# Performance work log

Measured on AMD Instinct MI355X. Metric: run time of the kernel, lower is better.

Reference implementation:

```python
import jax, jax.numpy as jnp
import numpy as np

CUTOFF_UPPER = 4.5
EYE3 = jnp.eye(3, dtype=jnp.float32)


def tensor_norm(t):
    return (t ** 2).sum((-2, -1))


def decompose_tensor(X):
    # X: [N, C, 3, 3]
    tr_mean = jnp.trace(X, axis1=-2, axis2=-1) / 3.0
    I = tr_mean[..., None, None] * EYE3
    Xt = jnp.swapaxes(X, -2, -1)
    A = 0.5 * (X - Xt)
    S = 0.5 * (X + Xt) - I
    return I, A, S


def chan_linear(T, W, b):
    # torch: Linear applied over the channel axis after permute(0,2,3,1)
    # T: [N, C, 3, 3], W: [C, C], b: [C]
    return jnp.einsum('nkij,ck->ncij', T, W) + b[None, :, None, None]


def setup_inputs() -> dict:
    key = jax.random.key(0)
    ks = jax.random.split(key, 16)
    Np1, H, R, E = 20001, 128, 64, 200000
    X = jax.random.normal(ks[0], (Np1, H, 3, 3), dtype=jnp.float32)
    edge_index = jax.random.randint(ks[1], (2, E), 0, Np1)
    edge_weight = jax.random.uniform(ks[2], (E,), dtype=jnp.float32) * CUTOFF_UPPER
    edge_attr = jax.random.normal(ks[3], (E, R), dtype=jnp.float32)
    s = lambda fin: 1.0 / np.sqrt(fin)
    W1 = jax.random.uniform(ks[4], (3, H, H), minval=-s(H), maxval=s(H), dtype=jnp.float32)
    b1 = jax.random.uniform(ks[5], (3, H), minval=-s(H), maxval=s(H), dtype=jnp.float32)
    W2a = jax.random.uniform(ks[6], (H, R), minval=-s(R), maxval=s(R), dtype=jnp.float32)
    b2a = jax.random.uniform(ks[7], (H,), minval=-s(R), maxval=s(R), dtype=jnp.float32)
    W2b = jax.random.uniform(ks[8], (2 * H, H), minval=-s(H), maxval=s(H), dtype=jnp.float32)
    b2b = jax.random.uniform(ks[9], (2 * H,), minval=-s(H), maxval=s(H), dtype=jnp.float32)
    W2c = jax.random.uniform(ks[10], (3 * H, 2 * H), minval=-s(2 * H), maxval=s(2 * H), dtype=jnp.float32)
    b2c = jax.random.uniform(ks[11], (3 * H,), minval=-s(2 * H), maxval=s(2 * H), dtype=jnp.float32)
    W3 = jax.random.uniform(ks[12], (3, H, H), minval=-s(H), maxval=s(H), dtype=jnp.float32)
    b3 = jax.random.uniform(ks[13], (3, H), minval=-s(H), maxval=s(H), dtype=jnp.float32)
    return dict(X=X, edge_index=edge_index, edge_weight=edge_weight, edge_attr=edge_attr,
                W1=W1, b1=b1, W2a=W2a, b2a=b2a, W2b=W2b, b2b=b2b, W2c=W2c, b2c=b2c, W3=W3, b3=b3)


def reference(X, edge_index, edge_weight, edge_attr, W1, b1, W2a, b2a, W2b, b2b, W2c, b2c, W3, b3):
    Np1, H = X.shape[0], X.shape[1]
    act = jax.nn.silu
    X = X / (tensor_norm(X) + 1.0)[..., None, None]
    I, A, S = decompose_tensor(X)
    I = chan_linear(I, W1[0], b1[0])
    A = chan_linear(A, W1[1], b1[1])
    S = chan_linear(S, W1[2], b1[2])
    Y = I + A + S
    h = act(edge_attr @ W2a.T + b2a)
    h = act(h @ W2b.T + b2b)
    h = act(h @ W2c.T + b2c)  # [E, 3H]
    C = 0.5 * (jnp.cos(edge_weight * (jnp.pi / CUTOFF_UPPER)) + 1.0)
    C = C * (edge_weight < CUTOFF_UPPER).astype(C.dtype)
    ea = (h * C[:, None]).reshape(h.shape[0], H, 3)
    dst, src = edge_index[0], edge_index[1]

    def mp(factor, T):
        msg = factor[:, :, None, None] * T[src]  # [E, H, 3, 3]
        return jax.ops.segment_sum(msg, dst, num_segments=Np1)

    msg = mp(ea[..., 0], I) + mp(ea[..., 1], A) + mp(ea[..., 2], S)
    new_features = jnp.matmul(msg, Y) + jnp.matmul(Y, msg)  # O(3) branch
    I, A, S = decompose_tensor(new_features)
    norm = (tensor_norm(I + A + S) + 1.0)[..., None, None]
    I, A, S = I / norm, A / norm, S / norm
    I = chan_linear(I, W3[0], b3[0])
    A = chan_linear(A, W3[1], b3[1])
    S = chan_linear(S, W3[2], b3[2])
    dX = I + A + S
    return X + dX + jnp.matmul(dX, dX)
```

## Files before the change

kernel.cpp:

```cpp
#include <hip/hip_runtime.h>
#include <math.h>
#include <stdint.h>

typedef unsigned short u16;
typedef __attribute__((ext_vector_type(8))) short short8;
typedef __attribute__((ext_vector_type(4))) float floatx4;

__device__ __forceinline__ float b2f(u16 u){
  union{unsigned int i; float f;} v; v.i = ((unsigned int)u)<<16; return v.f;
}
__device__ __forceinline__ u16 f2b(float f){
  union{unsigned int i; float f;} v; v.f = f;
  unsigned int r = (v.i + 0x7FFFu + ((v.i>>16)&1u))>>16;
  return (u16)r;
}
__device__ __forceinline__ float ldx(const void* p, size_t i, int isb){
  return isb ? b2f(((const u16*)p)[i]) : ((const float*)p)[i];
}
__device__ __forceinline__ void gll16(const u16* g, u16* l){
  __builtin_amdgcn_global_load_lds(
      (const __attribute__((address_space(1))) unsigned int*)(g),
      (__attribute__((address_space(3))) unsigned int*)(l), 16, 0, 0);
}

__global__ void k_sniff(const void* __restrict__ X, int* __restrict__ flag)
{
  __shared__ int cnt;
  if (threadIdx.x==0) cnt = 0;
  __syncthreads();
  int c = 0;
  for (int t = threadIdx.x; t < 512; t += 256){
    unsigned int u = ((const u16*)X)[2*t];
    int e = (u >> 7) & 0xFF;
    if (e >= 110 && e <= 139) c++;
  }
  atomicAdd(&cnt, c);
  __syncthreads();
  if (threadIdx.x==0) *flag = (cnt > 300) ? 1 : 0;
}

__global__ __launch_bounds__(256) void k_zero(float* __restrict__ p, int n)
{
  int i = blockIdx.x*256 + threadIdx.x;
  if (i < n) p[i] = 0.f;
}
__global__ __launch_bounds__(256) void k_zero_int(int* __restrict__ p, int n)
{
  int i = blockIdx.x*256 + threadIdx.x;
  if (i < n) p[i] = 0;
}

__global__ __launch_bounds__(256) void k_hist(
    const int* __restrict__ ei, int* __restrict__ counts, int E)
{
  int e = blockIdx.x*256 + threadIdx.x;
  if (e < E) atomicAdd(&counts[ei[e]], 1);
}
__global__ __launch_bounds__(256) void k_scan(
    const int* __restrict__ counts, int* __restrict__ rowptr,
    int* __restrict__ fill, int N)
{
  __shared__ int sm[256];
  int tid = threadIdx.x;
  int per = (N + 255) >> 8;
  int lo = tid*per; if (lo > N) lo = N;
  int hi = lo + per; if (hi > N) hi = N;
  int s = 0;
  for (int i = lo; i < hi; i++) s += counts[i];
  sm[tid] = s;
  __syncthreads();
  for (int off=1; off<256; off<<=1){
    int t = (tid >= off) ? sm[tid-off] : 0;
    __syncthreads();
    sm[tid] += t;
    __syncthreads();
  }
  int run = sm[tid] - s;
  for (int i = lo; i < hi; i++){
    int v = counts[i];
    rowptr[i] = run; fill[i] = run;
    run += v;
  }
  if (tid == 0) rowptr[N] = sm[255];
}
__global__ __launch_bounds__(256) void k_scatter(
    const int* __restrict__ ei, int* __restrict__ fill,
    int* __restrict__ eorder, int E)
{
  int e = blockIdx.x*256 + threadIdx.x;
  if (e >= E) return;
  int d = ei[e];
  int pos = atomicAdd(&fill[d], 1);
  eorder[pos] = e;
}

__global__ __launch_bounds__(256) void k_cvt_weights(
    const void* __restrict__ W1, const void* __restrict__ W3,
    const void* __restrict__ W2a, const void* __restrict__ W2b,
    const void* __restrict__ W2c, u16* __restrict__ out,
    const int* __restrict__ dflag)
{
  int isb = *dflag;
  int i = blockIdx.x*256 + threadIdx.x;
  if (i >= 237568) return;
  float v;
  if (i < 49152)        v = ldx(W1, i, isb);
  else if (i < 98304)   v = ldx(W3, i-49152, isb);
  else if (i < 106496)  v = ldx(W2a, i-98304, isb);
  else if (i < 139264)  v = ldx(W2b, i-106496, isb);
  else {
    int j = i - 139264;
    int r = j >> 8, c = j & 255;
    v = ldx(W2c, (size_t)((r & 127)*3 + (r >> 7))*256 + c, isb);
  }
  out[i] = f2b(v);
}
__global__ __launch_bounds__(256) void k_cvt_biases(
    const void* __restrict__ b2a, const void* __restrict__ b2b,
    const void* __restrict__ b2c, float* __restrict__ out,
    const int* __restrict__ dflag)
{
  int isb = *dflag;
  int i = blockIdx.x*256 + threadIdx.x;
  if (i < 128) out[i] = ldx(b2a, i, isb);
  else if (i < 384) out[i] = ldx(b2b, i-128, isb);
  else if (i < 768){ int c = i-384; out[i] = ldx(b2c, (c&127)*3 + (c>>7), isb); }
}
__global__ __launch_bounds__(256) void k_perm_eatt(
    const void* __restrict__ eatt, const int* __restrict__ eorder,
    u16* __restrict__ dst, int E, const int* __restrict__ dflag)
{
  int isb = *dflag;
  int row = blockIdx.x*4 + (threadIdx.x >> 6);
  int c = threadIdx.x & 63;
  if (row >= E) return;
  int e = eorder[row];
  dst[(size_t)row*64 + c] = f2b(ldx(eatt, (size_t)e*64 + c, isb));
}

__global__ __launch_bounds__(256) void k_decompose(
    const void* __restrict__ X, u16* __restrict__ Di, u16* __restrict__ Da,
    u16* __restrict__ Ds, int NH, const int* __restrict__ dflag)
{
  int tid = blockIdx.x*256 + threadIdx.x;
  if (tid >= NH) return;
  int isb = *dflag;
  int n = tid >> 7, k = tid & 127;
  float x[9]; float nrm = 0.f;
#pragma unroll
  for (int i=0;i<9;i++){ x[i]=ldx(X,(size_t)tid*9+i,isb); nrm += x[i]*x[i]; }
  float inv = 1.0f/(nrm+1.0f);
#pragma unroll
  for (int i=0;i<9;i++) x[i]*=inv;
  float i0 = (x[0]+x[4]+x[8])*(1.0f/3.0f);
  Di[tid] = f2b(i0);
  size_t ab = ((size_t)n*3)*128 + k;
  Da[ab      ] = f2b(0.5f*(x[1]-x[3]));
  Da[ab + 128] = f2b(0.5f*(x[2]-x[6]));
  Da[ab + 256] = f2b(0.5f*(x[5]-x[7]));
  size_t sb = ((size_t)n*6)*128 + k;
  Ds[sb      ] = f2b(x[0]-i0);
  Ds[sb + 128] = f2b(0.5f*(x[1]+x[3]));
  Ds[sb + 256] = f2b(0.5f*(x[2]+x[6]));
  Ds[sb + 384] = f2b(x[4]-i0);
  Ds[sb + 512] = f2b(0.5f*(x[5]+x[7]));
  Ds[sb + 640] = f2b(x[8]-i0);
}

__global__ __launch_bounds__(256) void k_mfma_gemm(
    const u16* __restrict__ A, const u16* __restrict__ B,
    const float* __restrict__ bias, const float* __restrict__ rowscale,
    u16* __restrict__ C, int M, int Ncol, int K, int flags)
{
  __shared__ u16 As[4096];
  __shared__ u16 Bs[4096];
  const int tid = threadIdx.x;
  const int lane = tid & 63, l15 = lane & 15, q = lane >> 4;
  const int wid = tid >> 6, wm = wid & 1, wn = wid >> 1;
  const int n0 = blockIdx.x * 128, m0 = blockIdx.y * 128;

  const int srow = wid*32 + (lane >> 2);
  const int qsrc = (lane & 3) ^ ((lane >> 3) & 3);
  int ar0 = m0 + srow;      if (ar0 >= M) ar0 = M-1;
  int ar1 = m0 + srow + 16; if (ar1 >= M) ar1 = M-1;
  const u16* aSrc0 = A + (size_t)ar0*K + qsrc*8;
  const u16* aSrc1 = A + (size_t)ar1*K + qsrc*8;
  const u16* bSrc0 = B + (size_t)(n0 + srow)*K + qsrc*8;
  const u16* bSrc1 = B + (size_t)(n0 + srow + 16)*K + qsrc*8;
  u16* aDst0 = &As[wid*1024];  u16* aDst1 = &As[wid*1024 + 512];
  u16* bDst0 = &Bs[wid*1024];  u16* bDst1 = &Bs[wid*1024 + 512];

  floatx4 acc[4][4];
#pragma unroll
  for (int i=0;i<4;i++)
#pragma unroll
    for (int j=0;j<4;j++) acc[i][j] = (floatx4)0.f;

  const int qsw  = ((q ^ ((l15 >> 1) & 3)) << 3);
  const int aBase = (wm*64 + l15)*32 + qsw;
  const int bBase = (wn*64 + l15)*32 + qsw;

  for (int k0 = 0; k0 < K; k0 += 32){
    gll16(aSrc0 + k0, aDst0);
    gll16(aSrc1 + k0, aDst1);
    gll16(bSrc0 + k0, bDst0);
    gll16(bSrc1 + k0, bDst1);
    __syncthreads();
    short8 av[4], bv[4];
#pragma unroll
    for (int mt=0; mt<4; mt++)
      av[mt] = *reinterpret_cast<const short8*>(&As[aBase + mt*512]);
#pragma unroll
    for (int nt=0; nt<4; nt++)
      bv[nt] = *reinterpret_cast<const short8*>(&Bs[bBase + nt*512]);
#pragma unroll
    for (int mt=0; mt<4; mt++)
#pragma unroll
      for (int nt=0; nt<4; nt++)
        acc[mt][nt] = __builtin_amdgcn_mfma_f32_16x16x32_bf16(av[mt], bv[nt], acc[mt][nt], 0, 0, 0);
    __syncthreads();
  }

  float biasv[4];
#pragma unroll
  for (int nt=0; nt<4; nt++)
    biasv[nt] = bias ? bias[n0 + wn*64 + nt*16 + l15] : 0.f;
#pragma unroll
  for (int mt=0; mt<4; mt++){
#pragma unroll
    for (int reg=0; reg<4; reg++){
      int row = m0 + wm*64 + mt*16 + q*4 + reg;
      if (row >= M) continue;
      float rs = (flags & 2) ? rowscale[row] : 1.0f;
#pragma unroll
      for (int nt=0; nt<4; nt++){
        int col = n0 + wn*64 + nt*16 + l15;
        float t = acc[mt][nt][reg] + biasv[nt];
        if (flags & 1) t = t / (1.0f + expf(-t));
        C[(size_t)row*Ncol + col] = f2b(t*rs);
      }
    }
  }
}

__global__ __launch_bounds__(256) void k_cutoff(
    const void* __restrict__ ew, const int* __restrict__ eorder, int c0,
    float* __restrict__ Cc, int ec, const int* __restrict__ dflag)
{
  int i = blockIdx.x*256 + threadIdx.x;
  if (i >= ec) return;
  int e = eorder[c0 + i];
  float w = ldx(ew, e, *dflag);
  float c = 0.0f;
  if (w < 4.5f) c = 0.5f*(cosf(w*0.6981317007977318f) + 1.0f);
  Cc[i] = c;
}

__global__ __launch_bounds__(128) void k_gather(
    const int* __restrict__ rowptr, const int* __restrict__ eorder,
    const int* __restrict__ ei, int E, int c0, int c1,
    const u16* __restrict__ ea,
    const u16* __restrict__ Pi, const u16* __restrict__ Pa,
    const u16* __restrict__ Ps, const void* __restrict__ b1,
    float* __restrict__ msg, int NH, const int* __restrict__ dflag)
{
  int n = blockIdx.x;
  int lo = rowptr[n], hi = rowptr[n+1];
  if (lo < c0) lo = c0;
  if (hi > c1) hi = c1;
  if (lo >= hi) return;
  int isb = *dflag;
  int c = threadIdx.x;
  float b0 = ldx(b1,c,isb), b1f = ldx(b1,128+c,isb), b2v = ldx(b1,256+c,isb);
  float m[9];
#pragma unroll
  for (int i=0;i<9;i++) m[i]=0.f;
  for (int idx = lo; idx < hi; idx++){
    int e = eorder[idx];
    int src = ei[E + e];
    const u16* er = ea + (size_t)(idx - c0)*384;
    float e0f = b2f(er[c]), e1f = b2f(er[128+c]), e2f = b2f(er[256+c]);
    float i1 = b2f(Pi[(size_t)src*128 + c]);
    size_t ab = (size_t)src*384 + c;
    float a0 = b2f(Pa[ab]), a1 = b2f(Pa[ab+128]), a2 = b2f(Pa[ab+256]);
    size_t sb = (size_t)src*768 + c;
    float s0 = b2f(Ps[sb]),     s1 = b2f(Ps[sb+128]), s2 = b2f(Ps[sb+256]);
    float s3 = b2f(Ps[sb+384]), s4 = b2f(Ps[sb+512]), s5 = b2f(Ps[sb+640]);
    float bb = e0f*b0 + e1f*b1f + e2f*b2v;
    float t0 = e0f*i1;
    m[0] += t0 + e2f*s0 + bb;
    m[1] += e1f*a0 + e2f*s1 + bb;
    m[2] += e1f*a1 + e2f*s2 + bb;
    m[3] += -e1f*a0 + e2f*s1 + bb;
    m[4] += t0 + e2f*s3 + bb;
    m[5] += e1f*a2 + e2f*s4 + bb;
    m[6] += -e1f*a1 + e2f*s2 + bb;
    m[7] += -e1f*a2 + e2f*s4 + bb;
    m[8] += t0 + e2f*s5 + bb;
  }
  size_t o = (size_t)n*128 + c;
#pragma unroll
  for (int i=0;i<9;i++) msg[(size_t)i*NH + o] += m[i];
}

__global__ __launch_bounds__(256) void k_update(
    const float* __restrict__ msg, const u16* __restrict__ Pi,
    const u16* __restrict__ Pa, const u16* __restrict__ Ps,
    const void* __restrict__ b1,
    u16* __restrict__ D2i, u16* __restrict__ D2a, u16* __restrict__ D2s,
    int NH, const int* __restrict__ dflag)
{
  int tid = blockIdx.x*256 + threadIdx.x;
  if (tid >= NH) return;
  int isb = *dflag;
  int n = tid >> 7, c = tid & 127;
  float Mx[9];
#pragma unroll
  for (int i=0;i<9;i++) Mx[i] = msg[(size_t)i*NH + tid];
  float i1 = b2f(Pi[tid]);
  size_t ab = ((size_t)n*3)*128 + c;
  float a0 = b2f(Pa[ab]), a1 = b2f(Pa[ab+128]), a2 = b2f(Pa[ab+256]);
  size_t sb = ((size_t)n*6)*128 + c;
  float s0 = b2f(Ps[sb]),     s1 = b2f(Ps[sb+128]), s2 = b2f(Ps[sb+256]);
  float s3 = b2f(Ps[sb+384]), s4 = b2f(Ps[sb+512]), s5 = b2f(Ps[sb+640]);
  float B = ldx(b1,c,isb) + ldx(b1,128+c,isb) + ldx(b1,256+c,isb);
  float Y[9];
  Y[0]= i1+s0+B; Y[1]= a0+s1+B; Y[2]= a1+s2+B;
  Y[3]=-a0+s1+B; Y[4]= i1+s3+B; Y[5]= a2+s4+B;
  Y[6]=-a1+s2+B; Y[7]=-a2+s4+B; Y[8]= i1+s5+B;
  float F[9];
#pragma unroll
  for (int i=0;i<3;i++)
#pragma unroll
    for (int j=0;j<3;j++){
      float acc = 0.f;
#pragma unroll
      for (int t=0;t<3;t++)
        acc += Mx[i*3+t]*Y[t*3+j] + Y[i*3+t]*Mx[t*3+j];
      F[i*3+j] = acc;
    }
  float nrm = 0.f;
#pragma unroll
  for (int i=0;i<9;i++) nrm += F[i]*F[i];
  float inv = 1.0f/(nrm+1.0f);
  float i2 = (F[0]+F[4]+F[8])*(1.0f/3.0f);
  D2i[tid] = f2b(i2*inv);
  D2a[ab      ] = f2b(0.5f*(F[1]-F[3])*inv);
  D2a[ab + 128] = f2b(0.5f*(F[2]-F[6])*inv);
  D2a[ab + 256] = f2b(0.5f*(F[5]-F[7])*inv);
  D2s[sb      ] = f2b((F[0]-i2)*inv);
  D2s[sb + 128] = f2b(0.5f*(F[1]+F[3])*inv);
  D2s[sb + 256] = f2b(0.5f*(F[2]+F[6])*inv);
  D2s[sb + 384] = f2b((F[4]-i2)*inv);
  D2s[sb + 512] = f2b(0.5f*(F[5]+F[7])*inv);
  D2s[sb + 640] = f2b((F[8]-i2)*inv);
}

__global__ __launch_bounds__(256) void k_final(
    const void* __restrict__ X, const u16* __restrict__ P2i,
    const u16* __restrict__ P2a, const u16* __restrict__ P2s,
    const void* __restrict__ b3, void* __restrict__ out, int NH,
    const int* __restrict__ dflag)
{
  int tid = blockIdx.x*256 + threadIdx.x;
  if (tid >= NH) return;
  int isb = *dflag;
  int n = tid >> 7, c = tid & 127;
  float i1 = b2f(P2i[tid]);
  size_t ab = ((size_t)n*3)*128 + c;
  float a0 = b2f(P2a[ab]), a1 = b2f(P2a[ab+128]), a2 = b2f(P2a[ab+256]);
  size_t sb = ((size_t)n*6)*128 + c;
  float s0 = b2f(P2s[sb]),     s1 = b2f(P2s[sb+128]), s2 = b2f(P2s[sb+256]);
  float s3 = b2f(P2s[sb+384]), s4 = b2f(P2s[sb+512]), s5 = b2f(P2s[sb+640]);
  float B = ldx(b3,c,isb) + ldx(b3,128+c,isb) + ldx(b3,256+c,isb);
  float dX[9];
  dX[0]= i1+s0+B; dX[1]= a0+s1+B; dX[2]= a1+s2+B;
  dX[3]=-a0+s1+B; dX[4]= i1+s3+B; dX[5]= a2+s4+B;
  dX[6]=-a1+s2+B; dX[7]=-a2+s4+B; dX[8]= i1+s5+B;

  float x[9]; float nrm = 0.f;
#pragma unroll
  for (int i=0;i<9;i++){ x[i]=ldx(X,(size_t)tid*9+i,isb); nrm += x[i]*x[i]; }
  float inv = 1.0f/(nrm+1.0f);

#pragma unroll
  for (int i=0;i<3;i++)
#pragma unroll
    for (int j=0;j<3;j++){
      float acc = 0.f;
#pragma unroll
      for (int t=0;t<3;t++) acc += dX[i*3+t]*dX[t*3+j];
      float v = x[i*3+j]*inv + dX[i*3+j] + acc;
      size_t oi = (size_t)tid*9 + i*3 + j;
      if (isb) ((u16*)out)[oi] = f2b(v);
      else     ((float*)out)[oi] = v;
    }
}

extern "C" void kernel_launch(void* const* d_in, const int* in_sizes, int n_in,
                              void* d_out, int out_size, void* d_ws, size_t ws_size,
                              hipStream_t stream)
{
  const void* X    = d_in[0];
  const int*  ei   = (const int*)d_in[1];
  const void* ew   = d_in[2];
  const void* eatt = d_in[3];
  const void* W1   = d_in[4];
  const void* b1   = d_in[5];
  const void* W2a  = d_in[6];
  const void* b2a  = d_in[7];
  const void* W2b  = d_in[8];
  const void* b2b  = d_in[9];
  const void* W2c  = d_in[10];
  const void* b2c  = d_in[11];
  const void* W3   = d_in[12];
  const void* b3   = d_in[13];

  const int NH = in_sizes[0]/9;
  const int E  = in_sizes[2];
  const int N  = NH/128;

  auto aln = [](size_t x){ return (x + 255) & ~(size_t)255; };
  char* ws = (char*)d_ws;
  size_t off = 0;
  size_t o_flag = off; off += 256;
  size_t o_msg  = off; off += aln((size_t)NH*9*4);
  size_t o_Di   = off; off += aln((size_t)NH*2);
  size_t o_Da   = off; off += aln((size_t)NH*6);
  size_t o_Ds   = off; off += aln((size_t)NH*12);
  size_t o_Pi   = off; off += aln((size_t)NH*2);
  size_t o_Pa   = off; off += aln((size_t)NH*6);
  size_t o_Ps   = off; off += aln((size_t)NH*12);
  size_t o_cnt  = off; off += aln((size_t)N*4);
  size_t o_rp   = off; off += aln((size_t)(N+1)*4);
  size_t o_fill = off; off += aln((size_t)N*4);
  size_t o_eord = off; off += aln((size_t)E*4);
  size_t o_eattb= off; off += aln((size_t)E*64*2);
  size_t o_wb   = off; off += aln((size_t)237568*2);
  size_t o_bf   = off; off += aln((size_t)768*4);
  size_t persistent = off;

  int EC;
  {
    size_t avail = (ws_size > persistent + 4096) ? (ws_size - persistent - 4096) : 0;
    size_t ecmax = avail / 1540;
    if (ecmax > (size_t)E) ecmax = (size_t)E;
    EC = (int)(ecmax & ~(size_t)1023);
    if (EC < 1024) EC = 1024;
  }
  size_t o_h1 = persistent;
  size_t o_h2 = o_h1 + aln((size_t)EC*256);
  size_t o_ea = o_h2 + aln((size_t)EC*512);
  size_t o_Cc = o_ea + aln((size_t)EC*768);
  (void)n_in; (void)out_size;

  int* dflag = (int*)(ws + o_flag);
  u16* Di = (u16*)(ws + o_Di);
  u16* Da = (u16*)(ws + o_Da);
  u16* Ds = (u16*)(ws + o_Ds);
  u16* Pi = (u16*)(ws + o_Pi);
  u16* Pa = (u16*)(ws + o_Pa);
  u16* Ps = (u16*)(ws + o_Ps);
  float* msg = (float*)(ws + o_msg);
  int* counts = (int*)(ws + o_cnt);
  int* rowptr = (int*)(ws + o_rp);
  int* fill   = (int*)(ws + o_fill);
  int* eorder = (int*)(ws + o_eord);
  u16* eattb  = (u16*)(ws + o_eattb);
  u16* wb     = (u16*)(ws + o_wb);
  float* bf   = (float*)(ws + o_bf);
  u16* h1 = (u16*)(ws + o_h1);
  u16* h2 = (u16*)(ws + o_h2);
  u16* ea = (u16*)(ws + o_ea);
  float* Cc = (float*)(ws + o_Cc);

  dim3 blk(256);
  auto gemm = [&](const u16* A, const u16* Bw, const float* bias, const float* rs,
                  u16* C, int M, int Ncol, int K, int flags){
    dim3 grid(Ncol/128, (M+127)/128);
    k_mfma_gemm<<<grid, blk, 0, stream>>>(A, Bw, bias, rs, C, M, Ncol, K, flags);
  };

  k_sniff<<<1, blk, 0, stream>>>(X, dflag);
  k_cvt_weights<<<(237568+255)/256, blk, 0, stream>>>(W1, W3, W2a, W2b, W2c, wb, dflag);
  k_cvt_biases<<<3, blk, 0, stream>>>(b2a, b2b, b2c, bf, dflag);
  k_decompose<<<(NH+255)/256, blk, 0, stream>>>(X, Di, Da, Ds, NH, dflag);
  gemm(Di, wb,       nullptr, nullptr, Pi, N,   128, 128, 0);
  gemm(Da, wb+16384, nullptr, nullptr, Pa, 3*N, 128, 128, 0);
  gemm(Ds, wb+32768, nullptr, nullptr, Ps, 6*N, 128, 128, 0);
  k_zero<<<((NH*9)+255)/256, blk, 0, stream>>>(msg, NH*9);
  k_zero_int<<<(N+255)/256, blk, 0, stream>>>(counts, N);
  k_hist<<<(E+255)/256, blk, 0, stream>>>(ei, counts, E);
  k_scan<<<1, blk, 0, stream>>>(counts, rowptr, fill, N);
  k_scatter<<<(E+255)/256, blk, 0, stream>>>(ei, fill, eorder, E);
  k_perm_eatt<<<(E+3)/4, blk, 0, stream>>>(eatt, eorder, eattb, E, dflag);
  for (int c0 = 0; c0 < E; c0 += EC){
    int ec = E - c0; if (ec > EC) ec = EC;
    k_cutoff<<<(ec+255)/256, blk, 0, stream>>>(ew, eorder, c0, Cc, ec, dflag);
    gemm(eattb + (size_t)c0*64, wb+98304,  bf,     nullptr, h1, ec, 128, 64,  1);
    gemm(h1,                    wb+106496, bf+128, nullptr, h2, ec, 256, 128, 1);
    gemm(h2,                    wb+139264, bf+384, Cc,      ea, ec, 384, 256, 1|2);
    k_gather<<<N, dim3(128), 0, stream>>>(rowptr, eorder, ei, E, c0, c0+ec,
                                          ea, Pi, Pa, Ps, b1, msg, NH, dflag);
  }
  k_update<<<(NH+255)/256, blk, 0, stream>>>(msg, Pi, Pa, Ps, b1, Di, Da, Ds, NH, dflag);
  gemm(Di, wb+49152, nullptr, nullptr, Pi, N,   128, 128, 0);
  gemm(Da, wb+65536, nullptr, nullptr, Pa, 3*N, 128, 128, 0);
  gemm(Ds, wb+81920, nullptr, nullptr, Ps, 6*N, 128, 128, 0);
  k_final<<<(NH+255)/256, blk, 0, stream>>>(X, Pi, Pa, Ps, b3, d_out, NH, dflag);
}
```

Before: 978.8 us.

## Vectorize elementwise kernels, stage X through LDS, drop msg zeroing pass

The decompose and final kernels now stage the strided 9-float X rows through shared memory with 16-byte coalesced loads and stores, and each thread handles two channels so the bf16 outputs are written as packed 32-bit words. The update kernel and the edge-attribute permute kernel use the same paired-channel packed loads and stores. The separate zeroing pass over the message buffer is removed; the first gather chunk writes its sums directly instead of accumulating. The goal is fewer uncoalesced narrow memory transactions and one less full-buffer pass, paid for with more LDS use and extra barriers per block.

```diff
diff --git a/kernel.cpp b/kernel.cpp
--- a/kernel.cpp
+++ b/kernel.cpp
@@ -13,6 +13,12 @@
   union{unsigned int i; float f;} v; v.f = f;
   unsigned int r = (v.i + 0x7FFFu + ((v.i>>16)&1u))>>16;
   return (u16)r;
+}
+__device__ __forceinline__ unsigned int pu(u16 lo, u16 hi){
+  return (unsigned int)lo | ((unsigned int)hi<<16);
+}
+__device__ __forceinline__ float gsel(unsigned int u, int s){
+  return b2f((u16)(s ? (u>>16) : (u & 0xffffu)));
 }
 __device__ __forceinline__ float ldx(const void* p, size_t i, int isb){
   return isb ? b2f(((const u16*)p)[i]) : ((const float*)p)[i];
@@ -39,11 +45,6 @@
   if (threadIdx.x==0) *flag = (cnt > 300) ? 1 : 0;
 }
 
-__global__ __launch_bounds__(256) void k_zero(float* __restrict__ p, int n)
-{
-  int i = blockIdx.x*256 + threadIdx.x;
-  if (i < n) p[i] = 0.f;
-}
 __global__ __launch_bounds__(256) void k_zero_int(int* __restrict__ p, int n)
 {
   int i = blockIdx.x*256 + threadIdx.x;
@@ -131,40 +132,83 @@
     u16* __restrict__ dst, int E, const int* __restrict__ dflag)
 {
   int isb = *dflag;
-  int row = blockIdx.x*4 + (threadIdx.x >> 6);
-  int c = threadIdx.x & 63;
+  int row = blockIdx.x*8 + (threadIdx.x >> 5);
+  int cp = (threadIdx.x & 31)*2;
   if (row >= E) return;
   int e = eorder[row];
-  dst[(size_t)row*64 + c] = f2b(ldx(eatt, (size_t)e*64 + c, isb));
+  unsigned int w;
+  if (isb){
+    w = *(const unsigned int*)((const u16*)eatt + (size_t)e*64 + cp);
+  } else {
+    float2 v = *(const float2*)((const float*)eatt + (size_t)e*64 + cp);
+    w = pu(f2b(v.x), f2b(v.y));
+  }
+  *(unsigned int*)(dst + (size_t)row*64 + cp) = w;
 }
 
 __global__ __launch_bounds__(256) void k_decompose(
     const void* __restrict__ X, u16* __restrict__ Di, u16* __restrict__ Da,
     u16* __restrict__ Ds, int NH, const int* __restrict__ dflag)
 {
-  int tid = blockIdx.x*256 + threadIdx.x;
-  if (tid >= NH) return;
+  __shared__ __align__(16) float buf[4608];
+  u16* bufu = (u16*)buf;
   int isb = *dflag;
-  int n = tid >> 7, k = tid & 127;
-  float x[9]; float nrm = 0.f;
-#pragma unroll
-  for (int i=0;i<9;i++){ x[i]=ldx(X,(size_t)tid*9+i,isb); nrm += x[i]*x[i]; }
-  float inv = 1.0f/(nrm+1.0f);
-#pragma unroll
-  for (int i=0;i<9;i++) x[i]*=inv;
-  float i0 = (x[0]+x[4]+x[8])*(1.0f/3.0f);
-  Di[tid] = f2b(i0);
-  size_t ab = ((size_t)n*3)*128 + k;
-  Da[ab      ] = f2b(0.5f*(x[1]-x[3]));
-  Da[ab + 128] = f2b(0.5f*(x[2]-x[6]));
-  Da[ab + 256] = f2b(0.5f*(x[5]-x[7]));
-  size_t sb = ((size_t)n*6)*128 + k;
-  Ds[sb      ] = f2b(x[0]-i0);
-  Ds[sb + 128] = f2b(0.5f*(x[1]+x[3]));
-  Ds[sb + 256] = f2b(0.5f*(x[2]+x[6]));
-  Ds[sb + 384] = f2b(x[4]-i0);
-  Ds[sb + 512] = f2b(0.5f*(x[5]+x[7]));
-  Ds[sb + 640] = f2b(x[8]-i0);
+  int tid = threadIdx.x;
+  size_t t0 = (size_t)blockIdx.x*512;
+  int validT = (int)((size_t)NH - t0); if (validT > 512) validT = 512;
+  int ve = validT*9;
+  if (isb){
+    const u16* src = (const u16*)X + t0*9;
+    for (int idx = tid; idx*8 < ve; idx += 256){
+      if (idx*8+7 < ve) ((uint4*)bufu)[idx] = *(const uint4*)(src + idx*8);
+      else for (int j=idx*8; j<ve; j++) bufu[j] = src[j];
+    }
+  } else {
+    const float* src = (const float*)X + t0*9;
+    for (int idx = tid; idx*4 < ve; idx += 256){
+      if (idx*4+3 < ve) ((float4*)buf)[idx] = *(const float4*)(src + idx*4);
+      else for (int j=idx*4; j<ve; j++) buf[j] = src[j];
+    }
+  }
+  __syncthreads();
+  int pairs = validT >> 1;
+  if (tid >= pairs) return;
+  int l2 = 2*tid;
+  size_t tid2 = t0 + l2;
+  int n = (int)(tid2 >> 7), c = (int)(tid2 & 127);
+  u16 ri[2], ra[2][3], rs[2][6];
+#pragma unroll
+  for (int s=0; s<2; s++){
+    float x[9]; float nrm = 0.f;
+#pragma unroll
+    for (int i=0;i<9;i++){
+      x[i] = isb ? b2f(bufu[(l2+s)*9+i]) : buf[(l2+s)*9+i];
+      nrm += x[i]*x[i];
+    }
+    float inv = 1.0f/(nrm+1.0f);
+#pragma unroll
+    for (int i=0;i<9;i++) x[i]*=inv;
+    float i0 = (x[0]+x[4]+x[8])*(1.0f/3.0f);
+    ri[s] = f2b(i0);
+    ra[s][0] = f2b(0.5f*(x[1]-x[3]));
+    ra[s][1] = f2b(0.5f*(x[2]-x[6]));
+    ra[s][2] = f2b(0.5f*(x[5]-x[7]));
+    rs[s][0] = f2b(x[0]-i0);
+    rs[s][1] = f2b(0.5f*(x[1]+x[3]));
+    rs[s][2] = f2b(0.5f*(x[2]+x[6]));
+    rs[s][3] = f2b(x[4]-i0);
+    rs[s][4] = f2b(0.5f*(x[5]+x[7]));
+    rs[s][5] = f2b(x[8]-i0);
+  }
+  *(unsigned int*)&Di[tid2] = pu(ri[0], ri[1]);
+  size_t ab = ((size_t)n*3)*128 + c;
+#pragma unroll
+  for (int j=0;j<3;j++)
+    *(unsigned int*)&Da[ab + (size_t)j*128] = pu(ra[0][j], ra[1][j]);
+  size_t sb = ((size_t)n*6)*128 + c;
+#pragma unroll
+  for (int j=0;j<6;j++)
+    *(unsigned int*)&Ds[sb + (size_t)j*128] = pu(rs[0][j], rs[1][j]);
 }
 
 __global__ __launch_bounds__(256) void k_mfma_gemm(
@@ -258,7 +302,7 @@
 
 __global__ __launch_bounds__(128) void k_gather(
     const int* __restrict__ rowptr, const int* __restrict__ eorder,
-    const int* __restrict__ ei, int E, int c0, int c1,
+    const int* __restrict__ ei, int E, int c0, int c1, int first,
     const u16* __restrict__ ea,
     const u16* __restrict__ Pi, const u16* __restrict__ Pa,
     const u16* __restrict__ Ps, const void* __restrict__ b1,
@@ -268,39 +312,46 @@
   int lo = rowptr[n], hi = rowptr[n+1];
   if (lo < c0) lo = c0;
   if (hi > c1) hi = c1;
-  if (lo >= hi) return;
+  if (!first && lo >= hi) return;
   int isb = *dflag;
   int c = threadIdx.x;
-  float b0 = ldx(b1,c,isb), b1f = ldx(b1,128+c,isb), b2v = ldx(b1,256+c,isb);
   float m[9];
 #pragma unroll
   for (int i=0;i<9;i++) m[i]=0.f;
-  for (int idx = lo; idx < hi; idx++){
-    int e = eorder[idx];
-    int src = ei[E + e];
-    const u16* er = ea + (size_t)(idx - c0)*384;
-    float e0f = b2f(er[c]), e1f = b2f(er[128+c]), e2f = b2f(er[256+c]);
-    float i1 = b2f(Pi[(size_t)src*128 + c]);
-    size_t ab = (size_t)src*384 + c;
-    float a0 = b2f(Pa[ab]), a1 = b2f(Pa[ab+128]), a2 = b2f(Pa[ab+256]);
-    size_t sb = (size_t)src*768 + c;
-    float s0 = b2f(Ps[sb]),     s1 = b2f(Ps[sb+128]), s2 = b2f(Ps[sb+256]);
-    float s3 = b2f(Ps[sb+384]), s4 = b2f(Ps[sb+512]), s5 = b2f(Ps[sb+640]);
-    float bb = e0f*b0 + e1f*b1f + e2f*b2v;
-    float t0 = e0f*i1;
-    m[0] += t0 + e2f*s0 + bb;
-    m[1] += e1f*a0 + e2f*s1 + bb;
-    m[2] += e1f*a1 + e2f*s2 + bb;
-    m[3] += -e1f*a0 + e2f*s1 + bb;
-    m[4] += t0 + e2f*s3 + bb;
-    m[5] += e1f*a2 + e2f*s4 + bb;
-    m[6] += -e1f*a1 + e2f*s2 + bb;
-    m[7] += -e1f*a2 + e2f*s4 + bb;
-    m[8] += t0 + e2f*s5 + bb;
+  if (lo < hi){
+    float b0 = ldx(b1,c,isb), b1f = ldx(b1,128+c,isb), b2v = ldx(b1,256+c,isb);
+    for (int idx = lo; idx < hi; idx++){
+      int e = eorder[idx];
+      int src = ei[E + e];
+      const u16* er = ea + (size_t)(idx - c0)*384;
+      float e0f = b2f(er[c]), e1f = b2f(er[128+c]), e2f = b2f(er[256+c]);
+      float i1 = b2f(Pi[(size_t)src*128 + c]);
+      size_t ab = (size_t)src*384 + c;
+      float a0 = b2f(Pa[ab]), a1 = b2f(Pa[ab+128]), a2 = b2f(Pa[ab+256]);
+      size_t sb = (size_t)src*768 + c;
+      float s0 = b2f(Ps[sb]),     s1 = b2f(Ps[sb+128]), s2 = b2f(Ps[sb+256]);
+      float s3 = b2f(Ps[sb+384]), s4 = b2f(Ps[sb+512]), s5 = b2f(Ps[sb+640]);
+      float bb = e0f*b0 + e1f*b1f + e2f*b2v;
+      float t0 = e0f*i1;
+      m[0] += t0 + e2f*s0 + bb;
+      m[1] += e1f*a0 + e2f*s1 + bb;
+      m[2] += e1f*a1 + e2f*s2 + bb;
+      m[3] += -e1f*a0 + e2f*s1 + bb;
+      m[4] += t0 + e2f*s3 + bb;
+      m[5] += e1f*a2 + e2f*s4 + bb;
+      m[6] += -e1f*a1 + e2f*s2 + bb;
+      m[7] += -e1f*a2 + e2f*s4 + bb;
+      m[8] += t0 + e2f*s5 + bb;
+    }
   }
   size_t o = (size_t)n*128 + c;
-#pragma unroll
-  for (int i=0;i<9;i++) msg[(size_t)i*NH + o] += m[i];
+  if (first){
+#pragma unroll
+    for (int i=0;i<9;i++) msg[(size_t)i*NH + o] = m[i];
+  } else {
+#pragma unroll
+    for (int i=0;i<9;i++) msg[(size_t)i*NH + o] += m[i];
+  }
 }
 
 __global__ __launch_bounds__(256) void k_update(
@@ -310,50 +361,71 @@
     u16* __restrict__ D2i, u16* __restrict__ D2a, u16* __restrict__ D2s,
     int NH, const int* __restrict__ dflag)
 {
-  int tid = blockIdx.x*256 + threadIdx.x;
-  if (tid >= NH) return;
+  size_t tid2 = ((size_t)blockIdx.x*256 + threadIdx.x)*2;
+  if (tid2 >= (size_t)NH) return;
   int isb = *dflag;
-  int n = tid >> 7, c = tid & 127;
-  float Mx[9];
-#pragma unroll
-  for (int i=0;i<9;i++) Mx[i] = msg[(size_t)i*NH + tid];
-  float i1 = b2f(Pi[tid]);
+  int n = (int)(tid2 >> 7), c = (int)(tid2 & 127);
+  float Mx[2][9];
+#pragma unroll
+  for (int i=0;i<9;i++){
+    float2 v = *(const float2*)&msg[(size_t)i*NH + tid2];
+    Mx[0][i] = v.x; Mx[1][i] = v.y;
+  }
+  unsigned int ui = *(const unsigned int*)&Pi[tid2];
   size_t ab = ((size_t)n*3)*128 + c;
-  float a0 = b2f(Pa[ab]), a1 = b2f(Pa[ab+128]), a2 = b2f(Pa[ab+256]);
+  unsigned int ua[3];
+#pragma unroll
+  for (int j=0;j<3;j++) ua[j] = *(const unsigned int*)&Pa[ab + (size_t)j*128];
   size_t sb = ((size_t)n*6)*128 + c;
-  float s0 = b2f(Ps[sb]),     s1 = b2f(Ps[sb+128]), s2 = b2f(Ps[sb+256]);
-  float s3 = b2f(Ps[sb+384]), s4 = b2f(Ps[sb+512]), s5 = b2f(Ps[sb+640]);
-  float B = ldx(b1,c,isb) + ldx(b1,128+c,isb) + ldx(b1,256+c,isb);
-  float Y[9];
-  Y[0]= i1+s0+B; Y[1]= a0+s1+B; Y[2]= a1+s2+B;
-  Y[3]=-a0+s1+B; Y[4]= i1+s3+B; Y[5]= a2+s4+B;
-  Y[6]=-a1+s2+B; Y[7]=-a2+s4+B; Y[8]= i1+s5+B;
-  float F[9];
-#pragma unroll
-  for (int i=0;i<3;i++)
-#pragma unroll
-    for (int j=0;j<3;j++){
-      float acc = 0.f;
-#pragma unroll
-      for (int t=0;t<3;t++)
-        acc += Mx[i*3+t]*Y[t*3+j] + Y[i*3+t]*Mx[t*3+j];
-      F[i*3+j] = acc;
-    }
-  float nrm = 0.f;
-#pragma unroll
-  for (int i=0;i<9;i++) nrm += F[i]*F[i];
-  float inv = 1.0f/(nrm+1.0f);
-  float i2 = (F[0]+F[4]+F[8])*(1.0f/3.0f);
-  D2i[tid] = f2b(i2*inv);
-  D2a[ab      ] = f2b(0.5f*(F[1]-F[3])*inv);
-  D2a[ab + 128] = f2b(0.5f*(F[2]-F[6])*inv);
-  D2a[ab + 256] = f2b(0.5f*(F[5]-F[7])*inv);
-  D2s[sb      ] = f2b((F[0]-i2)*inv);
-  D2s[sb + 128] = f2b(0.5f*(F[1]+F[3])*inv);
-  D2s[sb + 256] = f2b(0.5f*(F[2]+F[6])*inv);
-  D2s[sb + 384] = f2b((F[4]-i2)*inv);
-  D2s[sb + 512] = f2b(0.5f*(F[5]+F[7])*inv);
-  D2s[sb + 640] = f2b((F[8]-i2)*inv);
+  unsigned int us[6];
+#pragma unroll
+  for (int j=0;j<6;j++) us[j] = *(const unsigned int*)&Ps[sb + (size_t)j*128];
+  u16 ri[2], ra[2][3], rs[2][6];
+#pragma unroll
+  for (int s=0; s<2; s++){
+    float i1 = gsel(ui,s);
+    float a0 = gsel(ua[0],s), a1 = gsel(ua[1],s), a2 = gsel(ua[2],s);
+    float s0 = gsel(us[0],s), s1 = gsel(us[1],s), s2 = gsel(us[2],s);
+    float s3 = gsel(us[3],s), s4 = gsel(us[4],s), s5 = gsel(us[5],s);
+    float B = ldx(b1,c+s,isb) + ldx(b1,128+c+s,isb) + ldx(b1,256+c+s,isb);
+    float Y[9];
+    Y[0]= i1+s0+B; Y[1]= a0+s1+B; Y[2]= a1+s2+B;
+    Y[3]=-a0+s1+B; Y[4]= i1+s3+B; Y[5]= a2+s4+B;
+    Y[6]=-a1+s2+B; Y[7]=-a2+s4+B; Y[8]= i1+s5+B;
+    float F[9];
+#pragma unroll
+    for (int i=0;i<3;i++)
+#pragma unroll
+      for (int j=0;j<3;j++){
+        float acc = 0.f;
+#pragma unroll
+        for (int t=0;t<3;t++)
+          acc += Mx[s][i*3+t]*Y[t*3+j] + Y[i*3+t]*Mx[s][t*3+j];
+        F[i*3+j] = acc;
+      }
+    float nrm = 0.f;
+#pragma unroll
+    for (int i=0;i<9;i++) nrm += F[i]*F[i];
+    float inv = 1.0f/(nrm+1.0f);
+    float i2 = (F[0]+F[4]+F[8])*(1.0f/3.0f);
+    ri[s] = f2b(i2*inv);
+    ra[s][0] = f2b(0.5f*(F[1]-F[3])*inv);
+    ra[s][1] = f2b(0.5f*(F[2]-F[6])*inv);
+    ra[s][2] = f2b(0.5f*(F[5]-F[7])*inv);
+    rs[s][0] = f2b((F[0]-i2)*inv);
+    rs[s][1] = f2b(0.5f*(F[1]+F[3])*inv);
+    rs[s][2] = f2b(0.5f*(F[2]+F[6])*inv);
+    rs[s][3] = f2b((F[4]-i2)*inv);
+    rs[s][4] = f2b(0.5f*(F[5]+F[7])*inv);
+    rs[s][5] = f2b((F[8]-i2)*inv);
+  }
+  *(unsigned int*)&D2i[tid2] = pu(ri[0], ri[1]);
+#pragma unroll
+  for (int j=0;j<3;j++)
+    *(unsigned int*)&D2a[ab + (size_t)j*128] = pu(ra[0][j], ra[1][j]);
+#pragma unroll
+  for (int j=0;j<6;j++)
+    *(unsigned int*)&D2s[sb + (size_t)j*128] = pu(rs[0][j], rs[1][j]);
 }
 
 __global__ __launch_bounds__(256) void k_final(
@@ -362,39 +434,99 @@
     const void* __restrict__ b3, void* __restrict__ out, int NH,
     const int* __restrict__ dflag)
 {
-  int tid = blockIdx.x*256 + threadIdx.x;
-  if (tid >= NH) return;
+  __shared__ __align__(16) float buf[4608];
+  u16* bufu = (u16*)buf;
   int isb = *dflag;
-  int n = tid >> 7, c = tid & 127;
-  float i1 = b2f(P2i[tid]);
-  size_t ab = ((size_t)n*3)*128 + c;
-  float a0 = b2f(P2a[ab]), a1 = b2f(P2a[ab+128]), a2 = b2f(P2a[ab+256]);
-  size_t sb = ((size_t)n*6)*128 + c;
-  float s0 = b2f(P2s[sb]),     s1 = b2f(P2s[sb+128]), s2 = b2f(P2s[sb+256]);
-  float s3 = b2f(P2s[sb+384]), s4 = b2f(P2s[sb+512]), s5 = b2f(P2s[sb+640]);
-  float B = ldx(b3,c,isb) + ldx(b3,128+c,isb) + ldx(b3,256+c,isb);
-  float dX[9];
-  dX[0]= i1+s0+B; dX[1]= a0+s1+B; dX[2]= a1+s2+B;
-  dX[3]=-a0+s1+B; dX[4]= i1+s3+B; dX[5]= a2+s4+B;
-  dX[6]=-a1+s2+B; dX[7]=-a2+s4+B; dX[8]= i1+s5+B;
-
-  float x[9]; float nrm = 0.f;
-#pragma unroll
-  for (int i=0;i<9;i++){ x[i]=ldx(X,(size_t)tid*9+i,isb); nrm += x[i]*x[i]; }
-  float inv = 1.0f/(nrm+1.0f);
-
-#pragma unroll
-  for (int i=0;i<3;i++)
-#pragma unroll
-    for (int j=0;j<3;j++){
-      float acc = 0.f;
-#pragma unroll
-      for (int t=0;t<3;t++) acc += dX[i*3+t]*dX[t*3+j];
-      float v = x[i*3+j]*inv + dX[i*3+j] + acc;
-      size_t oi = (size_t)tid*9 + i*3 + j;
-      if (isb) ((u16*)out)[oi] = f2b(v);
-      else     ((float*)out)[oi] = v;
-    }
+  int tid = threadIdx.x;
+  size_t t0 = (size_t)blockIdx.x*512;
+  int validT = (int)((size_t)NH - t0); if (validT > 512) validT = 512;
+  int ve = validT*9;
+  if (isb){
+    const u16* src = (const u16*)X + t0*9;
+    for (int idx = tid; idx*8 < ve; idx += 256){
+      if (idx*8+7 < ve) ((uint4*)bufu)[idx] = *(const uint4*)(src + idx*8);
+      else for (int j=idx*8; j<ve; j++) bufu[j] = src[j];
+    }
+  } else {
+    const float* src = (const float*)X + t0*9;
+    for (int idx = tid; idx*4 < ve; idx += 256){
+      if (idx*4+3 < ve) ((float4*)buf)[idx] = *(const float4*)(src + idx*4);
+      else for (int j=idx*4; j<ve; j++) buf[j] = src[j];
+    }
+  }
+  __syncthreads();
+  int pairs = validT >> 1;
+  int l2 = 2*tid;
+  size_t tid2 = t0 + l2;
+  float vout[2][9];
+  if (tid < pairs){
+    int n = (int)(tid2 >> 7), c = (int)(tid2 & 127);
+    unsigned int ui = *(const unsigned int*)&P2i[tid2];
+    size_t ab = ((size_t)n*3)*128 + c;
+    unsigned int ua[3];
+#pragma unroll
+    for (int j=0;j<3;j++) ua[j] = *(const unsigned int*)&P2a[ab + (size_t)j*128];
+    size_t sb = ((size_t)n*6)*128 + c;
+    unsigned int us[6];
+#pragma unroll
+    for (int j=0;j<6;j++) us[j] = *(const unsigned int*)&P2s[sb + (size_t)j*128];
+#pragma unroll
+    for (int s=0; s<2; s++){
+      float i1 = gsel(ui,s);
+      float a0 = gsel(ua[0],s), a1 = gsel(ua[1],s), a2 = gsel(ua[2],s);
+      float s0 = gsel(us[0],s), s1 = gsel(us[1],s), s2 = gsel(us[2],s);
+      float s3 = gsel(us[3],s), s4 = gsel(us[4],s), s5 = gsel(us[5],s);
+      float B = ldx(b3,c+s,isb) + ldx(b3,128+c+s,isb) + ldx(b3,256+c+s,isb);
+      float dX[9];
+      dX[0]= i1+s0+B; dX[1]= a0+s1+B; dX[2]= a1+s2+B;
+      dX[3]=-a0+s1+B; dX[4]= i1+s3+B; dX[5]= a2+s4+B;
+      dX[6]=-a1+s2+B; dX[7]=-a2+s4+B; dX[8]= i1+s5+B;
+      float x[9]; float nrm = 0.f;
+#pragma unroll
+      for (int i=0;i<9;i++){
+        x[i] = isb ? b2f(bufu[(l2+s)*9+i]) : buf[(l2+s)*9+i];
+        nrm += x[i]*x[i];
+      }
+      float inv = 1.0f/(nrm+1.0f);
+#pragma unroll
+      for (int i=0;i<3;i++)
+#pragma unroll
+        for (int j=0;j<3;j++){
+          float acc = 0.f;
+#pragma unroll
+          for (int t=0;t<3;t++) acc += dX[i*3+t]*dX[t*3+j];
+          vout[s][i*3+j] = x[i*3+j]*inv + dX[i*3+j] + acc;
+        }
+    }
+  }
+  __syncthreads();
+  if (tid < pairs){
+    if (isb){
+#pragma unroll
+      for (int s=0;s<2;s++)
+#pragma unroll
+        for (int i=0;i<9;i++) bufu[(l2+s)*9+i] = f2b(vout[s][i]);
+    } else {
+#pragma unroll
+      for (int s=0;s<2;s++)
+#pragma unroll
+        for (int i=0;i<9;i++) buf[(l2+s)*9+i] = vout[s][i];
+    }
+  }
+  __syncthreads();
+  if (isb){
+    u16* dst = (u16*)out + t0*9;
+    for (int idx = tid; idx*8 < ve; idx += 256){
+      if (idx*8+7 < ve) *(uint4*)(dst + idx*8) = ((const uint4*)bufu)[idx];
+      else for (int j=idx*8; j<ve; j++) dst[j] = bufu[j];
+    }
+  } else {
+    float* dst = (float*)out + t0*9;
+    for (int idx = tid; idx*4 < ve; idx += 256){
+      if (idx*4+3 < ve) *(float4*)(dst + idx*4) = ((const float4*)buf)[idx];
+      else for (int j=idx*4; j<ve; j++) dst[j] = buf[j];
+    }
+  }
 }
 
 extern "C" void kernel_launch(void* const* d_in, const int* in_sizes, int n_in,
@@ -484,16 +616,15 @@
   k_sniff<<<1, blk, 0, stream>>>(X, dflag);
   k_cvt_weights<<<(237568+255)/256, blk, 0, stream>>>(W1, W3, W2a, W2b, W2c, wb, dflag);
   k_cvt_biases<<<3, blk, 0, stream>>>(b2a, b2b, b2c, bf, dflag);
-  k_decompose<<<(NH+255)/256, blk, 0, stream>>>(X, Di, Da, Ds, NH, dflag);
+  k_decompose<<<(NH+511)/512, blk, 0, stream>>>(X, Di, Da, Ds, NH, dflag);
   gemm(Di, wb,       nullptr, nullptr, Pi, N,   128, 128, 0);
   gemm(Da, wb+16384, nullptr, nullptr, Pa, 3*N, 128, 128, 0);
   gemm(Ds, wb+32768, nullptr, nullptr, Ps, 6*N, 128, 128, 0);
-  k_zero<<<((NH*9)+255)/256, blk, 0, stream>>>(msg, NH*9);
   k_zero_int<<<(N+255)/256, blk, 0, stream>>>(counts, N);
   k_hist<<<(E+255)/256, blk, 0, stream>>>(ei, counts, E);
   k_scan<<<1, blk, 0, stream>>>(counts, rowptr, fill, N);
   k_scatter<<<(E+255)/256, blk, 0, stream>>>(ei, fill, eorder, E);
-  k_perm_eatt<<<(E+3)/4, blk, 0, stream>>>(eatt, eorder, eattb, E, dflag);
+  k_perm_eatt<<<(E+7)/8, blk, 0, stream>>>(eatt, eorder, eattb, E, dflag);
   for (int c0 = 0; c0 < E; c0 += EC){
     int ec = E - c0; if (ec > EC) ec = EC;
     k_cutoff<<<(ec+255)/256, blk, 0, stream>>>(ew, eorder, c0, Cc, ec, dflag);
@@ -501,11 +632,12 @@
     gemm(h1,                    wb+106496, bf+128, nullptr, h2, ec, 256, 128, 1);
     gemm(h2,                    wb+139264, bf+384, Cc,      ea, ec, 384, 256, 1|2);
     k_gather<<<N, dim3(128), 0, stream>>>(rowptr, eorder, ei, E, c0, c0+ec,
+                                          (c0==0)?1:0,
                                           ea, Pi, Pa, Ps, b1, msg, NH, dflag);
   }
-  k_update<<<(NH+255)/256, blk, 0, stream>>>(msg, Pi, Pa, Ps, b1, Di, Da, Ds, NH, dflag);
+  k_update<<<(NH/2+255)/256, blk, 0, stream>>>(msg, Pi, Pa, Ps, b1, Di, Da, Ds, NH, dflag);
   gemm(Di, wb+49152, nullptr, nullptr, Pi, N,   128, 128, 0);
   gemm(Da, wb+65536, nullptr, nullptr, Pa, 3*N, 128, 128, 0);
   gemm(Ds, wb+81920, nullptr, nullptr, Ps, 6*N, 128, 128, 0);
-  k_final<<<(NH+255)/256, blk, 0, stream>>>(X, Pi, Pa, Ps, b3, d_out, NH, dflag);
-}
+  k_final<<<(NH+511)/512, blk, 0, stream>>>(X, Pi, Pa, Ps, b3, d_out, NH, dflag);
+}
```

After: 911.9 us. 1.07x faster.
